# Performance work log

Hardware: AMD Instinct MI355X
Metric: run time of the kernel (lower is better)

Reference implementation:

```python
import jax, jax.numpy as jnp
import numpy as np

N_MENTIONS = 4096
N_PAIRS = 32768
N_SEGMENTS = 1024  # number of spans (ragged softmax groups)
G_DIM = 3 * 768    # span representation dim (3*embed_dim)
D_IN = 3 * G_DIM + 20
HIDDEN = 150


def setup_inputs() -> dict:
    key = jax.random.key(0)
    ks = jax.random.split(key, 11)
    inp = {
        "g_i": jax.random.normal(ks[0], (N_MENTIONS, G_DIM), jnp.float32),
        "mention_scores": jax.random.normal(ks[1], (N_MENTIONS, 1), jnp.float32),
        "speaker_embed": jax.random.normal(ks[2], (3, 20), jnp.float32) * 0.02,
        "W1": jax.random.normal(ks[3], (D_IN, HIDDEN), jnp.float32) * (1.0 / np.sqrt(D_IN)),
        "b1": jnp.zeros((HIDDEN,), jnp.float32),
        "W2": jax.random.normal(ks[4], (HIDDEN, 1), jnp.float32) * (1.0 / np.sqrt(HIDDEN)),
        "b2": jnp.zeros((1,), jnp.float32),
        "mention_ids": jax.random.randint(ks[5], (N_PAIRS,), 0, N_MENTIONS),
        "antecedent_ids": jax.random.randint(ks[6], (N_PAIRS,), 0, N_MENTIONS),
        "speaker_labels": jax.random.randint(ks[7], (N_PAIRS,), 0, 3),
        "segment_ids": jnp.sort(jax.random.randint(ks[8], (N_PAIRS,), 0, N_SEGMENTS)),
    }
    return inp


def reference(g_i, mention_scores, speaker_embed, W1, b1, W2, b2,
              mention_ids, antecedent_ids, speaker_labels, segment_ids):
    # Gather mention / antecedent span representations. [P, G]
    i_g = g_i[mention_ids]
    j_g = g_i[antecedent_ids]
    phi = speaker_embed[speaker_labels]  # [P, speaker_dim]

    # Pair features: cat(i_g, j_g, i_g*j_g, phi). [P, D_IN]
    pairs = jnp.concatenate([i_g, j_g, i_g * j_g, phi], axis=1)

    # Score MLP: Linear -> ReLU -> Linear(->1). (dropout off in eval)
    h = jax.nn.relu(pairs @ W1 + b1)          # [P, HIDDEN]
    s_ij = (h @ W2 + b2)[:, 0]                # [P]

    # coref score = s_i + s_j + s_ij
    s_i = mention_scores[mention_ids, 0]
    s_j = mention_scores[antecedent_ids, 0]
    scores = s_i + s_j + s_ij                 # [P]

    # Ragged per-span softmax with an appended epsilon logit of 0.0.
    seg_max = jax.ops.segment_max(scores, segment_ids, num_segments=N_SEGMENTS)
    m = jnp.maximum(seg_max, 0.0)             # include epsilon=0 in the max
    e = jnp.exp(scores - m[segment_ids])      # [P]
    eps_e = jnp.exp(-m)                       # [S] exp(0 - m)
    denom = jax.ops.segment_sum(e, segment_ids, num_segments=N_SEGMENTS) + eps_e
    pair_probs = e / denom[segment_ids]       # [P]
    eps_probs = eps_e / denom                 # [S]

    # Flattened: all pair probs followed by the per-span epsilon probs.
    return jnp.concatenate([pair_probs, eps_probs])
```

## Files before the change

### kernel.cpp

```cpp
#include <hip/hip_runtime.h>
#include <cstdint>

#define NM   4096
#define NP   32768
#define NSEG 1024
#define GD   2304
#define HID  150
#define NPAD 160
#define KG32 72
#define SEG_ELEMS (KG32 * 10 * 512)

typedef unsigned short u16;
typedef short s16x8 __attribute__((ext_vector_type(8)));
typedef float f32x4 __attribute__((ext_vector_type(4)));
typedef uint32_t u32x4 __attribute__((ext_vector_type(4)));

union Frag {
    uint32_t u[4];
    s16x8    v;
};

__device__ inline uint32_t cvtpk(float lo, float hi) {
    uint32_t r;
    asm("v_cvt_pk_bf16_f32 %0, %1, %2" : "=v"(r) : "v"(lo), "v"(hi));
    return r;
}

__device__ inline f32x4 mfma16(s16x8 a, s16x8 b, f32x4 c) {
    return __builtin_amdgcn_mfma_f32_16x16x32_bf16(a, b, c, 0, 0, 0);
}

__device__ inline s16x8 prodpack(u32x4 iu, u32x4 ju) {
    Frag f;
#pragma unroll
    for (int m = 0; m < 4; ++m) {
        uint32_t x = iu[m], y = ju[m];
        float lo = __builtin_bit_cast(float, x << 16) *
                   __builtin_bit_cast(float, y << 16);
        float hi = __builtin_bit_cast(float, x & 0xffff0000u) *
                   __builtin_bit_cast(float, y & 0xffff0000u);
        f.u[m] = cvtpk(lo, hi);
    }
    return f.v;
}

__global__ void prep_pack_kernel(const float* __restrict__ W1,
                                 u16* __restrict__ wpack) {
    int idx = blockIdx.x * 256 + threadIdx.x;
    if (idx >= 3 * SEG_ELEMS) return;
    int segi = idx / SEG_ELEMS;
    int t    = idx - segi * SEG_ELEMS;
    int kg   = t / 5120;
    int r    = t - kg * 5120;
    int nf   = r >> 9;
    int q    = r & 511;
    int lane = q >> 3, j = q & 7;
    int kl = kg * 32 + ((lane >> 4) << 3) + j;
    int n  = nf * 16 + (lane & 15);
    int kbase = (segi == 0) ? 2 * GD : ((segi == 1) ? 0 : GD);
    float v = (n < HID) ? W1[(size_t)(kbase + kl) * HID + n] : 0.f;
    uint32_t a = __builtin_bit_cast(uint32_t, v);
    wpack[idx] = (u16)((a + 0x7fffu + ((a >> 16) & 1u)) >> 16);
}

__global__ void prep_tables_kernel(const float* __restrict__ spk,
                                   const float* __restrict__ W1,
                                   const float* __restrict__ b1,
                                   const float* __restrict__ W2,
                                   float* __restrict__ phib,
                                   float* __restrict__ w2pad) {
    int t = threadIdx.x;
    if (t < 3 * NPAD) {
        int s = t / NPAD, n = t - s * NPAD;
        float a = 0.f;
        if (n < HID) {
            for (int d = 0; d < 20; ++d)
                a = fmaf(spk[s * 20 + d], W1[(size_t)(3 * GD + d) * HID + n], a);
            a += b1[n];
        }
        phib[t] = a;
    } else if (t < 4 * NPAD) {
        int n = t - 3 * NPAD;
        w2pad[n] = (n < HID) ? W2[n] : 0.f;
    }
}

struct A2 { f32x4 x0, x1; };

__launch_bounds__(256)
__global__ void gemm_pre_kernel(const float* __restrict__ gi,
                                const u16* __restrict__ wpackIJ,
                                u16* __restrict__ gbf,
                                float* __restrict__ APre) {
    const int tid = threadIdx.x;
    const int kh = tid >> 6, lane = tid & 63;
    const int quad = lane >> 4, l15 = lane & 15;
    const int mt = blockIdx.x, ng = blockIdx.y;
    const u16* wp = wpackIJ + (size_t)ng * SEG_ELEMS + lane * 8;
    const int row = mt * 16 + l15;

    __shared__ float xch[3][64][44];

    f32x4 acc[10];
#pragma unroll
    for (int b = 0; b < 10; ++b) acc[b] = (f32x4){0.f, 0.f, 0.f, 0.f};

    const float* ap = gi + (size_t)row * GD + quad * 8;
    u16* gb = gbf + (size_t)row * GD + quad * 8;
    const bool emit = (ng == 0);
    const int u0 = kh * 18;

    A2 a0, a1, a2;
    Frag b0[10], b1[10];

#define LDA(ax, k) { ax.x0 = *(const f32x4*)(ap + (u0 + (k)) * 32); \
                     ax.x1 = *(const f32x4*)(ap + (u0 + (k)) * 32 + 4); }
#define LDBP(bb, k) { const u16* wn = wp + (size_t)(u0 + (k)) * 5120; \
        _Pragma("unroll") for (int nf = 0; nf < 10; ++nf) \
            bb[nf].v = *(const s16x8*)(const void*)(wn + nf * 512); }
#define PHP(k, ax, bb) { \
        Frag a; \
        a.u[0] = cvtpk(ax.x0[0], ax.x0[1]); a.u[1] = cvtpk(ax.x0[2], ax.x0[3]); \
        a.u[2] = cvtpk(ax.x1[0], ax.x1[1]); a.u[3] = cvtpk(ax.x1[2], ax.x1[3]); \
        if (emit) *(u32x4*)(gb + (u0 + (k)) * 32) = *(const u32x4*)a.u; \
        __builtin_amdgcn_s_setprio(1); \
        _Pragma("unroll") for (int nf = 0; nf < 10; ++nf) \
            acc[nf] = mfma16(a.v, bb[nf].v, acc[nf]); \
        __builtin_amdgcn_s_setprio(0); }

    LDA(a0, 0); LDA(a1, 1); LDA(a2, 2);
    LDBP(b0, 0); LDBP(b1, 1);

#pragma unroll 1
    for (int t = 0; t < 2; ++t) {
        const int kb = t * 6;
        PHP(kb + 0, a0, b0); LDA(a0, kb + 3); LDBP(b0, kb + 2);
        PHP(kb + 1, a1, b1); LDA(a1, kb + 4); LDBP(b1, kb + 3);
        PHP(kb + 2, a2, b0); LDA(a2, kb + 5); LDBP(b0, kb + 4);
        PHP(kb + 3, a0, b1); LDA(a0, kb + 6); LDBP(b1, kb + 5);
        PHP(kb + 4, a1, b0); LDA(a1, kb + 7); LDBP(b0, kb + 6);
        PHP(kb + 5, a2, b1); LDA(a2, kb + 8); LDBP(b1, kb + 7);
    }
    PHP(12, a0, b0); LDA(a0, 15); LDBP(b0, 14);
    PHP(13, a1, b1); LDA(a1, 16); LDBP(b1, 15);
    PHP(14, a2, b0); LDA(a2, 17); LDBP(b0, 16);
    PHP(15, a0, b1); LDBP(b1, 17);
    PHP(16, a1, b0);
    PHP(17, a2, b1);

#undef LDA
#undef LDBP
#undef PHP

    if (kh != 0) {
        float* dst = &xch[kh - 1][lane][0];
#pragma unroll
        for (int nf = 0; nf < 10; ++nf)
            *(f32x4*)(dst + nf * 4) = acc[nf];
    }
    __syncthreads();
    if (kh == 0) {
#pragma unroll
        for (int k = 0; k < 3; ++k) {
            const float* src = &xch[k][lane][0];
#pragma unroll
            for (int nf = 0; nf < 10; ++nf)
                acc[nf] += *(const f32x4*)(src + nf * 4);
        }
        const int colbase = ng * NPAD + l15;
        float* Ap = APre + (size_t)(mt * 16 + quad * 4) * 320 + colbase;
#pragma unroll
        for (int nf = 0; nf < 10; ++nf)
#pragma unroll
            for (int r = 0; r < 4; ++r)
                Ap[(size_t)r * 320 + nf * 16] = acc[nf][r];
    }
}

struct G4 { u32x4 i0, j0, i1, j1; };

__launch_bounds__(256)
__global__ void gemm_pairs_kernel(const u16* __restrict__ gbf,
                                  const u16* __restrict__ wpackP,
                                  const float* __restrict__ APre,
                                  const float* __restrict__ phib,
                                  const float* __restrict__ w2pad,
                                  const float* __restrict__ mscore,
                                  const float* __restrict__ b2,
                                  const int* __restrict__ mids,
                                  const int* __restrict__ aids,
                                  const int* __restrict__ slab,
                                  float* __restrict__ scores) {
    const int tid = threadIdx.x;
    const int w = tid >> 6, lane = tid & 63;
    const int pg = w >> 1, kh = w & 1;
    const int quad = lane >> 4, l15 = lane & 15;
    const int base = blockIdx.x * 64 + pg * 32;

    __shared__ float xch[2][64][84];

    f32x4 acc[2][10];
#pragma unroll
    for (int a = 0; a < 2; ++a)
#pragma unroll
        for (int b = 0; b < 10; ++b) acc[a][b] = (f32x4){0.f, 0.f, 0.f, 0.f};

    const int p0 = base + l15, p1 = base + 16 + l15;
    const u16* ip0 = gbf + (size_t)mids[p0] * GD + quad * 8;
    const u16* jp0 = gbf + (size_t)aids[p0] * GD + quad * 8;
    const u16* ip1 = gbf + (size_t)mids[p1] * GD + quad * 8;
    const u16* jp1 = gbf + (size_t)aids[p1] * GD + quad * 8;
    const int ko = kh * 36;
    const u16* wl = wpackP + (size_t)ko * 5120 + lane * 8;

    G4 g0, g1, g2;
    Frag b0[10], b1[10];

#define LDG(g, k) { const int off = (ko + (k)) * 32; \
        g.i0 = *(const u32x4*)(ip0 + off); g.j0 = *(const u32x4*)(jp0 + off); \
        g.i1 = *(const u32x4*)(ip1 + off); g.j1 = *(const u32x4*)(jp1 + off); }
#define LDB(bb, k) { const u16* wn = wl + (size_t)(k) * 5120; \
        _Pragma("unroll") for (int nf = 0; nf < 10; ++nf) \
            bb[nf].v = *(const s16x8*)(const void*)(wn + nf * 512); }
#define PH(k, g, bb) { \
        s16x8 a0 = prodpack(g.i0, g.j0); \
        s16x8 a1 = prodpack(g.i1, g.j1); \
        __builtin_amdgcn_s_setprio(1); \
        _Pragma("unroll") for (int nf = 0; nf < 10; ++nf) { \
            acc[0][nf] = mfma16(a0, bb[nf].v, acc[0][nf]); \
            acc[1][nf] = mfma16(a1, bb[nf].v, acc[1][nf]); } \
        __builtin_amdgcn_s_setprio(0); }

    LDG(g0, 0); LDG(g1, 1); LDG(g2, 2);
    LDB(b0, 0); LDB(b1, 1);

#pragma unroll 1
    for (int t = 0; t < 5; ++t) {
        const int kb = t * 6;
        PH(kb + 0, g0, b0); LDG(g0, kb + 3); LDB(b0, kb + 2);
        PH(kb + 1, g1, b1); LDG(g1, kb + 4); LDB(b1, kb + 3);
        PH(kb + 2, g2, b0); LDG(g2, kb + 5); LDB(b0, kb + 4);
        PH(kb + 3, g0, b1); LDG(g0, kb + 6); LDB(b1, kb + 5);
        PH(kb + 4, g1, b0); LDG(g1, kb + 7); LDB(b0, kb + 6);
        PH(kb + 5, g2, b1); LDG(g2, kb + 8); LDB(b1, kb + 7);
    }
    PH(30, g0, b0); LDG(g0, 33); LDB(b0, 32);
    PH(31, g1, b1); LDG(g1, 34); LDB(b1, 33);
    PH(32, g2, b0); LDG(g2, 35); LDB(b0, 34);
    PH(33, g0, b1); LDB(b1, 35);
    PH(34, g1, b0);
    PH(35, g2, b1);

#undef LDG
#undef LDB
#undef PH

    if (kh == 1) {
        float* dst = &xch[pg][lane][0];
#pragma unroll
        for (int mf = 0; mf < 2; ++mf)
#pragma unroll
            for (int nf = 0; nf < 10; ++nf)
                *(f32x4*)(dst + mf * 40 + nf * 4) = acc[mf][nf];
    }
    __syncthreads();
    if (kh == 1) return;

    {
        const float* src = &xch[pg][lane][0];
#pragma unroll
        for (int mf = 0; mf < 2; ++mf)
#pragma unroll
            for (int nf = 0; nf < 10; ++nf)
                acc[mf][nf] += *(const f32x4*)(src + mf * 40 + nf * 4);
    }

    float w2v[10];
#pragma unroll
    for (int nf = 0; nf < 10; ++nf) w2v[nf] = w2pad[nf * 16 + l15];
    const float b2v = b2[0];

#pragma unroll
    for (int mf = 0; mf < 2; ++mf)
#pragma unroll
        for (int r = 0; r < 4; ++r) {
            const int p  = base + mf * 16 + quad * 4 + r;
            const int mi = mids[p], ai = aids[p], sp = slab[p];
            const float* Ai = APre + (size_t)mi * 320;
            const float* Bj = APre + (size_t)ai * 320 + NPAD;
            const float* Ph = phib + sp * NPAD;
            float partial = 0.f;
#pragma unroll
            for (int nf = 0; nf < 10; ++nf) {
                const int c = nf * 16 + l15;
                float h = acc[mf][nf][r] + Ai[c] + Bj[c] + Ph[c];
                h = fmaxf(h, 0.f);
                partial = fmaf(h, w2v[nf], partial);
            }
            partial += __shfl_xor(partial, 1);
            partial += __shfl_xor(partial, 2);
            partial += __shfl_xor(partial, 4);
            partial += __shfl_xor(partial, 8);
            if (l15 == 0)
                scores[p] = partial + b2v + mscore[mi] + mscore[ai];
        }
}

__global__ void seg_softmax_kernel(const float* __restrict__ scores,
                                   const int* __restrict__ seg,
                                   float* __restrict__ out) {
    const int s = blockIdx.x;
    const int lane = threadIdx.x;
    int lo = 0, hi = NP;
    while (lo < hi) { int mid = (lo + hi) >> 1; if (seg[mid] < s) lo = mid + 1; else hi = mid; }
    const int start = lo;
    int lo2 = start, hi2 = NP;
    while (lo2 < hi2) { int mid = (lo2 + hi2) >> 1; if (seg[mid] <= s) lo2 = mid + 1; else hi2 = mid; }
    const int end = lo2;

    float m = 0.f;
    for (int i = start + lane; i < end; i += 64) m = fmaxf(m, scores[i]);
#pragma unroll
    for (int msk = 1; msk < 64; msk <<= 1) m = fmaxf(m, __shfl_xor(m, msk));

    float sum = 0.f;
    for (int i = start + lane; i < end; i += 64) sum += __expf(scores[i] - m);
#pragma unroll
    for (int msk = 1; msk < 64; msk <<= 1) sum += __shfl_xor(sum, msk);

    const float epse = __expf(-m);
    const float inv  = 1.f / (sum + epse);
    for (int i = start + lane; i < end; i += 64) out[i] = __expf(scores[i] - m) * inv;
    if (lane == 0) out[NP + s] = epse * inv;
}

extern "C" void kernel_launch(void* const* d_in, const int* in_sizes, int n_in,
                              void* d_out, int out_size, void* d_ws, size_t ws_size,
                              hipStream_t stream) {
    const float* gi     = (const float*)d_in[0];
    const float* mscore = (const float*)d_in[1];
    const float* spk    = (const float*)d_in[2];
    const float* W1     = (const float*)d_in[3];
    const float* b1     = (const float*)d_in[4];
    const float* W2     = (const float*)d_in[5];
    const float* b2     = (const float*)d_in[6];
    const int*   mids   = (const int*)d_in[7];
    const int*   aids   = (const int*)d_in[8];
    const int*   slab   = (const int*)d_in[9];
    const int*   segs   = (const int*)d_in[10];
    float* out = (float*)d_out;

    char* w = (char*)d_ws;
    u16*   gbf    = (u16*)w;
    u16*   wpack  = (u16*)(w + 18874368);
    float* APre   = (float*)(w + 21086208);
    float* scores = (float*)(w + 26329088);
    float* phib   = (float*)(w + 26460160);
    float* w2pad  = (float*)(w + 26462080);

    prep_pack_kernel<<<dim3((3 * SEG_ELEMS + 255) / 256), dim3(256), 0, stream>>>(W1, wpack);
    prep_tables_kernel<<<dim3(1), dim3(640), 0, stream>>>(spk, W1, b1, W2, phib, w2pad);
    gemm_pre_kernel<<<dim3(256, 2), dim3(256), 0, stream>>>(gi, wpack + SEG_ELEMS, gbf, APre);
    gemm_pairs_kernel<<<dim3(512), dim3(256), 0, stream>>>(gbf, wpack, APre, phib, w2pad,
                                                           mscore, b2, mids, aids, slab, scores);
    seg_softmax_kernel<<<dim3(NSEG), dim3(64), 0, stream>>>(scores, segs, out);
}
```

Measured before the change: 203.5 us.

## Drop split-K in pair GEMM, use 4-stage pipeline, vectorize weight packing

The pair GEMM kernel no longer splits K across two waves with an LDS reduction. Each wave now covers the full K range (72 steps) with a 4-deep gather pipeline at 128 threads per block, which removes the shared-memory exchange and barrier. The cost is fewer waves in flight overall and higher register pressure. The weight-pack prep kernel now writes 8 bf16 values per thread using a packed convert instead of one value per thread, and load issue order is changed in the pre-GEMM.

```diff
diff --git a/kernel.cpp b/kernel.cpp
--- a/kernel.cpp
+++ b/kernel.cpp
@@ -47,20 +47,25 @@
 __global__ void prep_pack_kernel(const float* __restrict__ W1,
                                  u16* __restrict__ wpack) {
     int idx = blockIdx.x * 256 + threadIdx.x;
-    if (idx >= 3 * SEG_ELEMS) return;
-    int segi = idx / SEG_ELEMS;
-    int t    = idx - segi * SEG_ELEMS;
-    int kg   = t / 5120;
-    int r    = t - kg * 5120;
-    int nf   = r >> 9;
-    int q    = r & 511;
-    int lane = q >> 3, j = q & 7;
-    int kl = kg * 32 + ((lane >> 4) << 3) + j;
-    int n  = nf * 16 + (lane & 15);
-    int kbase = (segi == 0) ? 2 * GD : ((segi == 1) ? 0 : GD);
-    float v = (n < HID) ? W1[(size_t)(kbase + kl) * HID + n] : 0.f;
-    uint32_t a = __builtin_bit_cast(uint32_t, v);
-    wpack[idx] = (u16)((a + 0x7fffu + ((a >> 16) & 1u)) >> 16);
+    if (idx >= 3 * KG32 * 10 * 64) return;
+    int lane = idx & 63;
+    int t    = idx >> 6;
+    int nf   = t % 10;
+    int sk   = t / 10;
+    int seg  = sk / KG32, kg = sk % KG32;
+    int kbase = (seg == 0) ? 2 * GD : ((seg == 1) ? 0 : GD);
+    int n    = nf * 16 + (lane & 15);
+    int krow = kbase + kg * 32 + ((lane >> 4) << 3);
+    u32x4 d = (u32x4){0u, 0u, 0u, 0u};
+    if (n < HID) {
+#pragma unroll
+        for (int jj = 0; jj < 4; ++jj) {
+            float v0 = W1[(size_t)(krow + 2 * jj) * HID + n];
+            float v1 = W1[(size_t)(krow + 2 * jj + 1) * HID + n];
+            d[jj] = cvtpk(v0, v1);
+        }
+    }
+    *(u32x4*)(wpack + (size_t)idx * 8) = d;
 }
 
 __global__ void prep_tables_kernel(const float* __restrict__ spk,
@@ -128,22 +133,22 @@
             acc[nf] = mfma16(a.v, bb[nf].v, acc[nf]); \
         __builtin_amdgcn_s_setprio(0); }
 
+    LDBP(b0, 0); LDBP(b1, 1);
     LDA(a0, 0); LDA(a1, 1); LDA(a2, 2);
-    LDBP(b0, 0); LDBP(b1, 1);
 
 #pragma unroll 1
     for (int t = 0; t < 2; ++t) {
         const int kb = t * 6;
-        PHP(kb + 0, a0, b0); LDA(a0, kb + 3); LDBP(b0, kb + 2);
-        PHP(kb + 1, a1, b1); LDA(a1, kb + 4); LDBP(b1, kb + 3);
-        PHP(kb + 2, a2, b0); LDA(a2, kb + 5); LDBP(b0, kb + 4);
-        PHP(kb + 3, a0, b1); LDA(a0, kb + 6); LDBP(b1, kb + 5);
-        PHP(kb + 4, a1, b0); LDA(a1, kb + 7); LDBP(b0, kb + 6);
-        PHP(kb + 5, a2, b1); LDA(a2, kb + 8); LDBP(b1, kb + 7);
-    }
-    PHP(12, a0, b0); LDA(a0, 15); LDBP(b0, 14);
-    PHP(13, a1, b1); LDA(a1, 16); LDBP(b1, 15);
-    PHP(14, a2, b0); LDA(a2, 17); LDBP(b0, 16);
+        PHP(kb + 0, a0, b0); LDBP(b0, kb + 2); LDA(a0, kb + 3);
+        PHP(kb + 1, a1, b1); LDBP(b1, kb + 3); LDA(a1, kb + 4);
+        PHP(kb + 2, a2, b0); LDBP(b0, kb + 4); LDA(a2, kb + 5);
+        PHP(kb + 3, a0, b1); LDBP(b1, kb + 5); LDA(a0, kb + 6);
+        PHP(kb + 4, a1, b0); LDBP(b0, kb + 6); LDA(a1, kb + 7);
+        PHP(kb + 5, a2, b1); LDBP(b1, kb + 7); LDA(a2, kb + 8);
+    }
+    PHP(12, a0, b0); LDBP(b0, 14); LDA(a0, 15);
+    PHP(13, a1, b1); LDBP(b1, 15); LDA(a1, 16);
+    PHP(14, a2, b0); LDBP(b0, 16); LDA(a2, 17);
     PHP(15, a0, b1); LDBP(b1, 17);
     PHP(16, a1, b0);
     PHP(17, a2, b1);
@@ -179,7 +184,7 @@
 
 struct G4 { u32x4 i0, j0, i1, j1; };
 
-__launch_bounds__(256)
+__launch_bounds__(128)
 __global__ void gemm_pairs_kernel(const u16* __restrict__ gbf,
                                   const u16* __restrict__ wpackP,
                                   const float* __restrict__ APre,
@@ -192,12 +197,9 @@
                                   const int* __restrict__ slab,
                                   float* __restrict__ scores) {
     const int tid = threadIdx.x;
-    const int w = tid >> 6, lane = tid & 63;
-    const int pg = w >> 1, kh = w & 1;
+    const int wave = tid >> 6, lane = tid & 63;
     const int quad = lane >> 4, l15 = lane & 15;
-    const int base = blockIdx.x * 64 + pg * 32;
-
-    __shared__ float xch[2][64][84];
+    const int base = blockIdx.x * 64 + wave * 32;
 
     f32x4 acc[2][10];
 #pragma unroll
@@ -210,19 +212,18 @@
     const u16* jp0 = gbf + (size_t)aids[p0] * GD + quad * 8;
     const u16* ip1 = gbf + (size_t)mids[p1] * GD + quad * 8;
     const u16* jp1 = gbf + (size_t)aids[p1] * GD + quad * 8;
-    const int ko = kh * 36;
-    const u16* wl = wpackP + (size_t)ko * 5120 + lane * 8;
-
-    G4 g0, g1, g2;
+    const u16* wl = wpackP + lane * 8;
+
+    G4 g0, g1, g2, g3;
     Frag b0[10], b1[10];
 
-#define LDG(g, k) { const int off = (ko + (k)) * 32; \
+#define LDG(g, k) { const int off = (k) * 32; \
         g.i0 = *(const u32x4*)(ip0 + off); g.j0 = *(const u32x4*)(jp0 + off); \
         g.i1 = *(const u32x4*)(ip1 + off); g.j1 = *(const u32x4*)(jp1 + off); }
 #define LDB(bb, k) { const u16* wn = wl + (size_t)(k) * 5120; \
         _Pragma("unroll") for (int nf = 0; nf < 10; ++nf) \
             bb[nf].v = *(const s16x8*)(const void*)(wn + nf * 512); }
-#define PH(k, g, bb) { \
+#define PH(g, bb) { \
         s16x8 a0 = prodpack(g.i0, g.j0); \
         s16x8 a1 = prodpack(g.i1, g.j1); \
         __builtin_amdgcn_s_setprio(1); \
@@ -231,49 +232,25 @@
             acc[1][nf] = mfma16(a1, bb[nf].v, acc[1][nf]); } \
         __builtin_amdgcn_s_setprio(0); }
 
-    LDG(g0, 0); LDG(g1, 1); LDG(g2, 2);
     LDB(b0, 0); LDB(b1, 1);
+    LDG(g0, 0); LDG(g1, 1); LDG(g2, 2); LDG(g3, 3);
 
 #pragma unroll 1
-    for (int t = 0; t < 5; ++t) {
-        const int kb = t * 6;
-        PH(kb + 0, g0, b0); LDG(g0, kb + 3); LDB(b0, kb + 2);
-        PH(kb + 1, g1, b1); LDG(g1, kb + 4); LDB(b1, kb + 3);
-        PH(kb + 2, g2, b0); LDG(g2, kb + 5); LDB(b0, kb + 4);
-        PH(kb + 3, g0, b1); LDG(g0, kb + 6); LDB(b1, kb + 5);
-        PH(kb + 4, g1, b0); LDG(g1, kb + 7); LDB(b0, kb + 6);
-        PH(kb + 5, g2, b1); LDG(g2, kb + 8); LDB(b1, kb + 7);
-    }
-    PH(30, g0, b0); LDG(g0, 33); LDB(b0, 32);
-    PH(31, g1, b1); LDG(g1, 34); LDB(b1, 33);
-    PH(32, g2, b0); LDG(g2, 35); LDB(b0, 34);
-    PH(33, g0, b1); LDB(b1, 35);
-    PH(34, g1, b0);
-    PH(35, g2, b1);
+    for (int t = 0; t < 17; ++t) {
+        const int kb = t * 4;
+        PH(g0, b0); LDB(b0, kb + 2); LDG(g0, kb + 4);
+        PH(g1, b1); LDB(b1, kb + 3); LDG(g1, kb + 5);
+        PH(g2, b0); LDB(b0, kb + 4); LDG(g2, kb + 6);
+        PH(g3, b1); LDB(b1, kb + 5); LDG(g3, kb + 7);
+    }
+    PH(g0, b0); LDB(b0, 70);
+    PH(g1, b1); LDB(b1, 71);
+    PH(g2, b0);
+    PH(g3, b1);
 
 #undef LDG
 #undef LDB
 #undef PH
-
-    if (kh == 1) {
-        float* dst = &xch[pg][lane][0];
-#pragma unroll
-        for (int mf = 0; mf < 2; ++mf)
-#pragma unroll
-            for (int nf = 0; nf < 10; ++nf)
-                *(f32x4*)(dst + mf * 40 + nf * 4) = acc[mf][nf];
-    }
-    __syncthreads();
-    if (kh == 1) return;
-
-    {
-        const float* src = &xch[pg][lane][0];
-#pragma unroll
-        for (int mf = 0; mf < 2; ++mf)
-#pragma unroll
-            for (int nf = 0; nf < 10; ++nf)
-                acc[mf][nf] += *(const f32x4*)(src + mf * 40 + nf * 4);
-    }
 
     float w2v[10];
 #pragma unroll
@@ -358,10 +335,10 @@
     float* phib   = (float*)(w + 26460160);
     float* w2pad  = (float*)(w + 26462080);
 
-    prep_pack_kernel<<<dim3((3 * SEG_ELEMS + 255) / 256), dim3(256), 0, stream>>>(W1, wpack);
+    prep_pack_kernel<<<dim3((3 * KG32 * 10 * 64 + 255) / 256), dim3(256), 0, stream>>>(W1, wpack);
     prep_tables_kernel<<<dim3(1), dim3(640), 0, stream>>>(spk, W1, b1, W2, phib, w2pad);
     gemm_pre_kernel<<<dim3(256, 2), dim3(256), 0, stream>>>(gi, wpack + SEG_ELEMS, gbf, APre);
-    gemm_pairs_kernel<<<dim3(512), dim3(256), 0, stream>>>(gbf, wpack, APre, phib, w2pad,
+    gemm_pairs_kernel<<<dim3(512), dim3(128), 0, stream>>>(gbf, wpack, APre, phib, w2pad,
                                                            mscore, b2, mids, aids, slab, scores);
     seg_softmax_kernel<<<dim3(NSEG), dim3(64), 0, stream>>>(scores, segs, out);
 }
```

After: 193.1 us. 1.05x faster.
